# Performance work log

Measured on AMD Instinct MI355X. Metric: run time of the kernel, lower is better.

Reference implementation:

```python
import jax, jax.numpy as jnp
import numpy as np

B_AUDIOS = 64      # num audios in batch
NODES    = 2048    # 5-frame chunks (nodes) per audio
IN, HID, OUT = 512, 256, 128
HEADS, NCLS  = 2, 7
NEG_SLOPE = 0.2    # PyG GATConv default


def setup_inputs() -> dict:
    key = jax.random.key(0)
    ks = jax.random.split(key, 12)
    N = B_AUDIOS * NODES
    # chain edges within each audio: i -> i+1 (local), offset per audio
    base = np.arange(NODES - 1)
    src = (base[None, :] + np.arange(B_AUDIOS)[:, None] * NODES).reshape(-1)
    edge_index = jnp.asarray(np.stack([src, src + 1]), dtype=jnp.int32)
    batch_indices = jnp.repeat(jnp.arange(B_AUDIOS, dtype=jnp.int32), NODES)
    s = 0.05
    return {
        "x": jax.random.normal(ks[0], (N, IN), jnp.float32),
        "edge_index": edge_index,
        "batch_indices": batch_indices,
        "num_audios": B_AUDIOS,
        "W1": jax.random.normal(ks[1], (HEADS * HID, IN)) * s,
        "as1": jax.random.normal(ks[2], (HEADS, HID)) * s,
        "ad1": jax.random.normal(ks[3], (HEADS, HID)) * s,
        "b1": jnp.zeros((HID,), jnp.float32),
        "W2": jax.random.normal(ks[4], (HEADS * OUT, HID)) * s,
        "as2": jax.random.normal(ks[5], (HEADS, OUT)) * s,
        "ad2": jax.random.normal(ks[6], (HEADS, OUT)) * s,
        "b2": jnp.zeros((OUT,), jnp.float32),
        "Wt": jax.random.normal(ks[7], (1, OUT)) * s,
        "bt": jnp.zeros((1,), jnp.float32),
        "Wa": jax.random.normal(ks[8], (2, OUT)) * s,
        "ba": jnp.zeros((2,), jnp.float32),
        "Wn": jax.random.normal(ks[9], (NCLS, OUT)) * s,
        "bn": jnp.zeros((NCLS,), jnp.float32),
    }


def _seg_softmax(e, seg, n):
    m = jax.ops.segment_max(e, seg, num_segments=n)
    ex = jnp.exp(e - m[seg])
    return ex / jax.ops.segment_sum(ex, seg, num_segments=n)[seg]


def _gat_conv(x, src, dst, W, a_src, a_dst, b):
    # PyG GATConv, heads=H, concat=False (head-mean), with self loops
    N = x.shape[0]
    H, C = a_src.shape
    loops = jnp.arange(N, dtype=src.dtype)
    s = jnp.concatenate([src, loops])
    d = jnp.concatenate([dst, loops])
    h = (x @ W.T).reshape(N, H, C)                      # [N,H,C]
    al_s = jnp.einsum('nhc,hc->nh', h, a_src)           # [N,H]
    al_d = jnp.einsum('nhc,hc->nh', h, a_dst)
    e = jax.nn.leaky_relu(al_s[s] + al_d[d], NEG_SLOPE)  # [E,H]
    alpha = _seg_softmax(e, d, N)                        # softmax over in-edges of dst
    out = jax.ops.segment_sum(alpha[:, :, None] * h[s], d, num_segments=N)
    return out.mean(axis=1) + b                          # concat=False -> head mean


def reference(x, edge_index, batch_indices, num_audios,
              W1, as1, ad1, b1, W2, as2, ad2, b2,
              Wt, bt, Wa, ba, Wn, bn):
    src, dst = edge_index[0], edge_index[1]
    # global GAT (gat1 -> relu -> gat2)
    h1 = jax.nn.relu(_gat_conv(x, src, dst, W1, as1, ad1, b1))
    emb = _gat_conv(h1, src, dst, W2, as2, ad2, b2)      # [N, OUT]
    node_pred = jax.nn.softmax(emb @ Wn.T + bn, axis=-1)
    # per-audio subgraph GAT: graphs are disjoint per-audio chains, so running the
    # same GATModel on each subgraph equals restricting the global embeddings.
    logit = (emb @ Wt.T + bt)[:, 0]                      # [N]
    w = _seg_softmax(logit, batch_indices, num_audios)   # per-audio temporal softmax
    attended = jax.ops.segment_sum(w[:, None] * emb, batch_indices,
                                   num_segments=num_audios)  # [B, OUT]
    audio_pred = attended @ Wa.T + ba                    # [B, 2]
    return node_pred, audio_pred
```

## Files before the change

### kernel.cpp

```cpp
#include <hip/hip_runtime.h>
#include <hip/hip_bf16.h>

typedef __bf16 bf16x8 __attribute__((ext_vector_type(8)));
typedef float f32x4 __attribute__((ext_vector_type(4)));

#define NTOT   131072
#define NODES_PER_AUDIO 2048
#define NAUDIO 64
#define POOL_CHUNKS 16
#define CHUNK_NODES (NODES_PER_AUDIO / POOL_CHUNKS)

__global__ __launch_bounds__(256)
void detect_dtype(const unsigned* __restrict__ x, int* __restrict__ flag)
{
    const int tid = threadIdx.x;
    int cnt = 0;
    for (int i = tid; i < 4096; i += 256) {
        unsigned e = (x[i] >> 7) & 0xFF;
        cnt += (e >= 100 && e <= 145) ? 1 : 0;
    }
    __shared__ int red[256];
    red[tid] = cnt; __syncthreads();
    for (int s = 128; s > 0; s >>= 1) {
        if (tid < s) red[tid] += red[tid + s];
        __syncthreads();
    }
    if (tid == 0) *flag = (red[0] > 3000) ? 1 : 0;
}

struct W14 { const void* s[14]; int n[14]; int off[14]; };

__global__ __launch_bounds__(256)
void convert_weights(W14 w, const int* __restrict__ flag, __bf16* __restrict__ wb)
{
    const int f = *flag;
    const int stride = gridDim.x * 256;
    for (int t = 0; t < 14; t++) {
        const void* src = w.s[t];
        __bf16* d = wb + w.off[t];
        for (int i = blockIdx.x * 256 + threadIdx.x; i < w.n[t]; i += stride)
            d[i] = f ? ((const __bf16*)src)[i] : (__bf16)((const float*)src)[i];
    }
}

template<int NX, bool DYN>
__global__ __launch_bounds__(256)
void gemm_tile(const void* __restrict__ Araw, const __bf16* __restrict__ W,
               __bf16* __restrict__ C, int M, int K, int Nc,
               const int* __restrict__ flagp)
{
    __shared__ __align__(16) __bf16 As[128 * 64];
    __shared__ __align__(16) __bf16 Bs[128 * 64];

    const int nb  = gridDim.x;
    const int ny  = nb / NX;
    const int ypx = ny >> 3;
    const int bid = blockIdx.x;
    const int xcd = bid & 7;
    const int local = bid >> 3;
    const int by = xcd * ypx + local / NX;
    const int bx = local % NX;

    const int colBase = bx * 128;
    const int rowBase = by * 128;
    const int tid  = threadIdx.x;
    const int wave = tid >> 6;
    const int lane = tid & 63;
    const int wrow = (wave >> 1) * 64;
    const int wcol = (wave & 1) * 64;
    const int lr = lane & 15;
    const int lq = lane >> 4;
    int f = 1;
    if constexpr (DYN) f = *flagp;

    f32x4 acc[4][4] = {};

    const __bf16* A16 = (const __bf16*)Araw;
    const float*  A32 = (const float*)Araw;
    const __bf16* ap[4]; const float* af32[4]; const __bf16* bp[4];
    #pragma unroll
    for (int i = 0; i < 4; i++) {
        const int c = tid + 256 * i;
        const int r = c >> 3, q = c & 7;
        ap[i]   = A16 + (size_t)(rowBase + r) * K + q * 8;
        af32[i] = A32 + (size_t)(rowBase + r) * K + q * 8;
        bp[i]   = W   + (size_t)(colBase + r) * K + q * 8;
    }

    for (int k0 = 0; k0 < K; k0 += 64) {
        __syncthreads();
        #pragma unroll
        for (int i = 0; i < 4; i++) {
            const int c = tid + 256 * i;
            __builtin_amdgcn_global_load_lds(
                (const __attribute__((address_space(1))) void*)(bp[i] + k0),
                (__attribute__((address_space(3))) void*)&Bs[c * 8], 16, 0, 0);
        }
        if (!DYN || f) {
            #pragma unroll
            for (int i = 0; i < 4; i++) {
                const int c = tid + 256 * i;
                __builtin_amdgcn_global_load_lds(
                    (const __attribute__((address_space(1))) void*)(ap[i] + k0),
                    (__attribute__((address_space(3))) void*)&As[c * 8], 16, 0, 0);
            }
        } else {
            #pragma unroll
            for (int i = 0; i < 4; i++) {
                const int c = tid + 256 * i;
                float4 u0 = *(const float4*)(af32[i] + k0);
                float4 u1 = *(const float4*)(af32[i] + k0 + 4);
                __bf16 t[8] = {(__bf16)u0.x, (__bf16)u0.y, (__bf16)u0.z, (__bf16)u0.w,
                               (__bf16)u1.x, (__bf16)u1.y, (__bf16)u1.z, (__bf16)u1.w};
                *(int4*)&As[c * 8] = *(int4*)t;
            }
        }
        __syncthreads();

        #pragma unroll
        for (int kk = 0; kk < 2; kk++) {
            bf16x8 avf[4], bvf[4];
            #pragma unroll
            for (int i = 0; i < 4; i++)
                avf[i] = *(const bf16x8*)&As[(wrow + i * 16 + lr) * 64 + kk * 32 + lq * 8];
            #pragma unroll
            for (int j = 0; j < 4; j++)
                bvf[j] = *(const bf16x8*)&Bs[(wcol + j * 16 + lr) * 64 + kk * 32 + lq * 8];
            #pragma unroll
            for (int i = 0; i < 4; i++)
                #pragma unroll
                for (int j = 0; j < 4; j++)
                    acc[i][j] = __builtin_amdgcn_mfma_f32_16x16x32_bf16(
                        avf[i], bvf[j], acc[i][j], 0, 0, 0);
        }
    }

    #pragma unroll
    for (int i = 0; i < 4; i++) {
        #pragma unroll
        for (int j = 0; j < 4; j++) {
            int col = colBase + wcol + j * 16 + lr;
            #pragma unroll
            for (int r = 0; r < 4; r++) {
                int row = rowBase + wrow + i * 16 + lq * 4 + r;
                C[(size_t)row * Nc + col] = (__bf16)acc[i][j][r];
            }
        }
    }
}

template<int C, bool RELU, bool FUSE_HEAD>
__global__ __launch_bounds__(256)
void agg_fused(const __bf16* __restrict__ h, const __bf16* __restrict__ a_s,
               const __bf16* __restrict__ a_d, const __bf16* __restrict__ bias,
               void* __restrict__ outv,
               const __bf16* __restrict__ Wn, const __bf16* __restrict__ bn,
               const __bf16* __restrict__ Wt, const __bf16* __restrict__ bt,
               void* __restrict__ node_pred, float* __restrict__ logit,
               const int* __restrict__ flag)
{
    constexpr int D = 2 * C;
    constexpr int V = D / 64;
    const int n = blockIdx.x * 4 + (threadIdx.x >> 6);
    const int lane = threadIdx.x & 63;
    const bool have_prev = (n & (NODES_PER_AUDIO - 1)) != 0;
    const size_t np = have_prev ? (size_t)(n - 1) : (size_t)n;
    const int base = lane * V;

    __bf16 h0v[V], h1v[V];
    if constexpr (V == 8) {
        *(int4*)h0v = *(const int4*)(h + (size_t)n * D + base);
        *(int4*)h1v = *(const int4*)(h + np * D + base);
    } else {
        *(int2*)h0v = *(const int2*)(h + (size_t)n * D + base);
        *(int2*)h1v = *(const int2*)(h + np * D + base);
    }

    float ps = 0.f, pd = 0.f, pp = 0.f;
    #pragma unroll
    for (int j = 0; j < V; j++) {
        float av = (float)a_s[base + j], dv = (float)a_d[base + j];
        float x0 = (float)h0v[j], x1 = (float)h1v[j];
        ps += x0 * av; pd += x0 * dv; pp += x1 * av;
    }
    #pragma unroll
    for (int off = 1; off < 32; off <<= 1) {
        ps += __shfl_xor(ps, off, 64);
        pd += __shfl_xor(pd, off, 64);
        pp += __shfl_xor(pp, off, 64);
    }

    float es = ps + pd;  es = es > 0.f ? es : 0.2f * es;
    float a_self = 1.f, a_prev = 0.f;
    if (have_prev) {
        float ep = pp + pd;  ep = ep > 0.f ? ep : 0.2f * ep;
        float m = fmaxf(es, ep);
        float wsx = __expf(es - m), wpx = __expf(ep - m);
        float inv = 1.f / (wsx + wpx);
        a_self = wsx * inv; a_prev = wpx * inv;
    }

    const int cb = (lane & 31) * V;
    float outj[V];
    #pragma unroll
    for (int j = 0; j < V; j++) {
        float p = a_self * (float)h0v[j] + a_prev * (float)h1v[j];
        p = 0.5f * (p + __shfl_xor(p, 32, 64));
        p += (float)bias[cb + j];
        if (RELU) p = fmaxf(p, 0.f);
        outj[j] = p;
    }

    if constexpr (!FUSE_HEAD) {
        if (lane < 32) {
            __bf16 ov[V];
            #pragma unroll
            for (int j = 0; j < V; j++) ov[j] = (__bf16)outj[j];
            if constexpr (V == 8)
                *(int4*)((__bf16*)outv + (size_t)n * C + cb) = *(int4*)ov;
            else
                *(int2*)((__bf16*)outv + (size_t)n * C + cb) = *(int2*)ov;
        }
    } else {
        if (lane < 32)
            *(float4*)((float*)outv + (size_t)n * C + cb) = *(float4*)outj;

        float acc[8];
        #pragma unroll
        for (int k = 0; k < 7; k++) {
            float a = 0.f;
            #pragma unroll
            for (int j = 0; j < V; j++)
                a += outj[j] * (float)Wn[k * C + cb + j];
            acc[k] = a;
        }
        {
            float a = 0.f;
            #pragma unroll
            for (int j = 0; j < V; j++)
                a += outj[j] * (float)Wt[cb + j];
            acc[7] = a;
        }
        #pragma unroll
        for (int off = 1; off < 32; off <<= 1)
            #pragma unroll
            for (int k = 0; k < 8; k++)
                acc[k] += __shfl_xor(acc[k], off, 64);

        if (lane == 0) {
            float lg[7], m = -1e30f;
            #pragma unroll
            for (int k = 0; k < 7; k++) {
                lg[k] = acc[k] + (float)bn[k];
                m = fmaxf(m, lg[k]);
            }
            float s = 0.f;
            #pragma unroll
            for (int k = 0; k < 7; k++) { lg[k] = __expf(lg[k] - m); s += lg[k]; }
            float inv = 1.f / s;
            if (*flag) {
                #pragma unroll
                for (int k = 0; k < 7; k++)
                    ((__bf16*)node_pred)[(size_t)n * 7 + k] = (__bf16)(lg[k] * inv);
            } else {
                #pragma unroll
                for (int k = 0; k < 7; k++)
                    ((float*)node_pred)[(size_t)n * 7 + k] = lg[k] * inv;
            }
            logit[n] = acc[7] + (float)bt[0];
        }
    }
}

__global__ __launch_bounds__(256)
void audio_stats(const float* __restrict__ logit, float2* __restrict__ stats)
{
    const int b = blockIdx.x;
    const int tid = threadIdx.x;
    __shared__ float red[256];
    const float* lg = logit + b * NODES_PER_AUDIO;

    float m = -1e30f;
    for (int i = tid; i < NODES_PER_AUDIO; i += 256) m = fmaxf(m, lg[i]);
    red[tid] = m; __syncthreads();
    for (int s = 128; s > 0; s >>= 1) {
        if (tid < s) red[tid] = fmaxf(red[tid], red[tid + s]);
        __syncthreads();
    }
    m = red[0]; __syncthreads();

    float s = 0.f;
    for (int i = tid; i < NODES_PER_AUDIO; i += 256) s += __expf(lg[i] - m);
    red[tid] = s; __syncthreads();
    for (int st = 128; st > 0; st >>= 1) {
        if (tid < st) red[tid] += red[tid + st];
        __syncthreads();
    }
    if (tid == 0) stats[b] = make_float2(m, 1.f / red[0]);
}

__global__ __launch_bounds__(256)
void audio_partial(const float* __restrict__ emb, const float* __restrict__ logit,
                   const float2* __restrict__ stats, float* __restrict__ partial)
{
    const int b = blockIdx.x >> 4;
    const int chunk = blockIdx.x & 15;
    const int tid = threadIdx.x;
    const int c = tid & 127, half = tid >> 7;
    const float m = stats[b].x, inv = stats[b].y;
    const float* lg = logit + b * NODES_PER_AUDIO;
    const float* eb = emb + (size_t)b * NODES_PER_AUDIO * 128;

    __shared__ float attbuf[256];
    const int n0 = chunk * CHUNK_NODES + half * (CHUNK_NODES / 2);
    float att = 0.f;
    for (int i = n0; i < n0 + CHUNK_NODES / 2; i++) {
        float w = __expf(lg[i] - m) * inv;
        att += w * eb[(size_t)i * 128 + c];
    }
    attbuf[tid] = att; __syncthreads();
    if (tid < 128)
        partial[(size_t)(b * POOL_CHUNKS + chunk) * 128 + tid] =
            attbuf[tid] + attbuf[tid + 128];
}

__global__ __launch_bounds__(64)
void audio_final(const float* __restrict__ partial, const __bf16* __restrict__ Wa,
                 const __bf16* __restrict__ ba, void* __restrict__ outbase,
                 const int* __restrict__ flag)
{
    const int b = blockIdx.x;
    const int lane = threadIdx.x;
    const float* pb = partial + (size_t)b * POOL_CHUNKS * 128;

    float a0 = 0.f, a1 = 0.f;
    #pragma unroll
    for (int k = 0; k < POOL_CHUNKS; k++) {
        a0 += pb[k * 128 + lane * 2];
        a1 += pb[k * 128 + lane * 2 + 1];
    }
    float p0 = a0 * (float)Wa[lane * 2]       + a1 * (float)Wa[lane * 2 + 1];
    float p1 = a0 * (float)Wa[128 + lane * 2] + a1 * (float)Wa[128 + lane * 2 + 1];
    #pragma unroll
    for (int off = 1; off < 64; off <<= 1) {
        p0 += __shfl_xor(p0, off, 64);
        p1 += __shfl_xor(p1, off, 64);
    }
    if (lane == 0) {
        float r0 = p0 + (float)ba[0];
        float r1 = p1 + (float)ba[1];
        if (*flag) {
            ((__bf16*)outbase)[(size_t)NTOT * 7 + b * 2 + 0] = (__bf16)r0;
            ((__bf16*)outbase)[(size_t)NTOT * 7 + b * 2 + 1] = (__bf16)r1;
        } else {
            ((float*)outbase)[(size_t)NTOT * 7 + b * 2 + 0] = r0;
            ((float*)outbase)[(size_t)NTOT * 7 + b * 2 + 1] = r1;
        }
    }
}

extern "C" void kernel_launch(void* const* d_in, const int* in_sizes, int n_in,
                              void* d_out, int out_size, void* d_ws, size_t ws_size,
                              hipStream_t stream)
{
    const void* x = d_in[0];
    char* ws = (char*)d_ws;
    const size_t N = NTOT;

    __bf16* h  = (__bf16*)ws;
    size_t off = N * 1024;
    __bf16* h1 = (__bf16*)(ws + off); off += N * 512;
    float* logit = (float*)(ws + off); off += N * 4;
    __bf16* wb = (__bf16*)(ws + off); off += 331008 * 2;
    int* flag = (int*)(ws + off); off += 16;
    float2* stats = (float2*)(ws + off); off += NAUDIO * sizeof(float2);
    float* partial = (float*)(ws + off); off += (size_t)NAUDIO * POOL_CHUNKS * 128 * 4;
    __bf16* g2 = h;
    float* emb = (float*)(ws + N * 512);

    const int O_W1 = 0,      O_W2 = 262144, O_as1 = 327680, O_ad1 = 328192;
    const int O_b1 = 328704, O_as2 = 328960, O_ad2 = 329216, O_b2 = 329472;
    const int O_Wt = 329600, O_bt = 329728, O_Wa = 329736, O_ba = 329992;
    const int O_Wn = 330000, O_bn = 330896;

    W14 w;
    const void* srcs[14] = { d_in[4], d_in[8], d_in[5], d_in[6], d_in[7],
                             d_in[9], d_in[10], d_in[11], d_in[12], d_in[13],
                             d_in[14], d_in[15], d_in[16], d_in[17] };
    const int ns[14]   = { 262144, 65536, 512, 512, 256, 256, 256, 128,
                           128, 1, 256, 2, 896, 7 };
    const int offs[14] = { O_W1, O_W2, O_as1, O_ad1, O_b1, O_as2, O_ad2, O_b2,
                           O_Wt, O_bt, O_Wa, O_ba, O_Wn, O_bn };
    for (int i = 0; i < 14; i++) { w.s[i] = srcs[i]; w.n[i] = ns[i]; w.off[i] = offs[i]; }

    const int nwb = NTOT / 4;

    detect_dtype<<<1, 256, 0, stream>>>((const unsigned*)x, flag);
    convert_weights<<<512, 256, 0, stream>>>(w, flag, wb);

    gemm_tile<4, true><<<4 * (NTOT / 128), 256, 0, stream>>>(
        x, wb + O_W1, h, NTOT, 512, 512, flag);
    agg_fused<256, true, false><<<nwb, 256, 0, stream>>>(
        h, wb + O_as1, wb + O_ad1, wb + O_b1, h1,
        nullptr, nullptr, nullptr, nullptr, nullptr, nullptr, flag);
    gemm_tile<2, false><<<2 * (NTOT / 128), 256, 0, stream>>>(
        h1, wb + O_W2, g2, NTOT, 256, 256, flag);
    agg_fused<128, false, true><<<nwb, 256, 0, stream>>>(
        g2, wb + O_as2, wb + O_ad2, wb + O_b2, emb,
        wb + O_Wn, wb + O_bn, wb + O_Wt, wb + O_bt, d_out, logit, flag);
    audio_stats<<<NAUDIO, 256, 0, stream>>>(logit, stats);
    audio_partial<<<NAUDIO * POOL_CHUNKS, 256, 0, stream>>>(emb, logit, stats, partial);
    audio_final<<<NAUDIO, 64, 0, stream>>>(partial, wb + O_Wa, wb + O_ba, d_out, flag);
}
```

Baseline: 649.5 us.

## Double-buffer GEMM tiles via register staging with XOR-swizzled LDS layout

```diff
diff --git a/kernel.cpp b/kernel.cpp
--- a/kernel.cpp
+++ b/kernel.cpp
@@ -45,12 +45,12 @@
 
 template<int NX, bool DYN>
 __global__ __launch_bounds__(256)
-void gemm_tile(const void* __restrict__ Araw, const __bf16* __restrict__ W,
-               __bf16* __restrict__ C, int M, int K, int Nc,
-               const int* __restrict__ flagp)
-{
-    __shared__ __align__(16) __bf16 As[128 * 64];
-    __shared__ __align__(16) __bf16 Bs[128 * 64];
+void gemm_rs(const void* __restrict__ Araw, const __bf16* __restrict__ W,
+             __bf16* __restrict__ C, int M, int K, int Nc,
+             const int* __restrict__ flagp)
+{
+    __shared__ __align__(16) __bf16 As[2 * 128 * 64];
+    __shared__ __align__(16) __bf16 Bs[2 * 128 * 64];
 
     const int nb  = gridDim.x;
     const int ny  = nb / NX;
@@ -60,80 +60,89 @@
     const int local = bid >> 3;
     const int by = xcd * ypx + local / NX;
     const int bx = local % NX;
-
-    const int colBase = bx * 128;
-    const int rowBase = by * 128;
+    const int rowBase = by * 128, colBase = bx * 128;
+
     const int tid  = threadIdx.x;
-    const int wave = tid >> 6;
-    const int lane = tid & 63;
-    const int wrow = (wave >> 1) * 64;
-    const int wcol = (wave & 1) * 64;
-    const int lr = lane & 15;
-    const int lq = lane >> 4;
+    const int wave = tid >> 6, lane = tid & 63;
+    const int wrow = (wave >> 1) * 64, wcol = (wave & 1) * 64;
+    const int lr = lane & 15, lq = lane >> 4;
     int f = 1;
     if constexpr (DYN) f = *flagp;
 
-    f32x4 acc[4][4] = {};
-
     const __bf16* A16 = (const __bf16*)Araw;
     const float*  A32 = (const float*)Araw;
-    const __bf16* ap[4]; const float* af32[4]; const __bf16* bp[4];
+
+    const __bf16* apB[4]; const float* apF[4]; const __bf16* bpB[4]; int ld[4];
     #pragma unroll
     for (int i = 0; i < 4; i++) {
-        const int c = tid + 256 * i;
-        const int r = c >> 3, q = c & 7;
-        ap[i]   = A16 + (size_t)(rowBase + r) * K + q * 8;
-        af32[i] = A32 + (size_t)(rowBase + r) * K + q * 8;
-        bp[i]   = W   + (size_t)(colBase + r) * K + q * 8;
-    }
-
-    for (int k0 = 0; k0 < K; k0 += 64) {
-        __syncthreads();
-        #pragma unroll
-        for (int i = 0; i < 4; i++) {
-            const int c = tid + 256 * i;
-            __builtin_amdgcn_global_load_lds(
-                (const __attribute__((address_space(1))) void*)(bp[i] + k0),
-                (__attribute__((address_space(3))) void*)&Bs[c * 8], 16, 0, 0);
-        }
-        if (!DYN || f) {
-            #pragma unroll
-            for (int i = 0; i < 4; i++) {
-                const int c = tid + 256 * i;
-                __builtin_amdgcn_global_load_lds(
-                    (const __attribute__((address_space(1))) void*)(ap[i] + k0),
-                    (__attribute__((address_space(3))) void*)&As[c * 8], 16, 0, 0);
-            }
-        } else {
-            #pragma unroll
-            for (int i = 0; i < 4; i++) {
-                const int c = tid + 256 * i;
-                float4 u0 = *(const float4*)(af32[i] + k0);
-                float4 u1 = *(const float4*)(af32[i] + k0 + 4);
-                __bf16 t[8] = {(__bf16)u0.x, (__bf16)u0.y, (__bf16)u0.z, (__bf16)u0.w,
-                               (__bf16)u1.x, (__bf16)u1.y, (__bf16)u1.z, (__bf16)u1.w};
-                *(int4*)&As[c * 8] = *(int4*)t;
-            }
-        }
-        __syncthreads();
+        const int c = tid + 256 * i, r = c >> 3, q = (c & 7) ^ (r & 7);
+        apB[i] = A16 + (size_t)(rowBase + r) * K + q * 8;
+        apF[i] = A32 + (size_t)(rowBase + r) * K + q * 8;
+        bpB[i] = W   + (size_t)(colBase + r) * K + q * 8;
+        ld[i]  = c * 8;
+    }
+
+    f32x4 acc[4][4] = {};
+    const int NS = K >> 6;
+    int4 sa[4], sb[4];
+
+    #define LOADR(S) do {                                                     \
+        const int _k0 = (S) * 64;                                             \
+        _Pragma("unroll")                                                     \
+        for (int _i = 0; _i < 4; _i++) {                                      \
+            if (!DYN || f) {                                                  \
+                sa[_i] = *(const int4*)(apB[_i] + _k0);                       \
+            } else {                                                          \
+                float4 u0 = *(const float4*)(apF[_i] + _k0);                  \
+                float4 u1 = *(const float4*)(apF[_i] + _k0 + 4);              \
+                __bf16 t[8] = {(__bf16)u0.x, (__bf16)u0.y, (__bf16)u0.z,      \
+                               (__bf16)u0.w, (__bf16)u1.x, (__bf16)u1.y,      \
+                               (__bf16)u1.z, (__bf16)u1.w};                   \
+                sa[_i] = *(const int4*)t;                                     \
+            }                                                                 \
+            sb[_i] = *(const int4*)(bpB[_i] + _k0);                           \
+        } } while (0)
+
+    #define WRITER(P) do {                                                    \
+        _Pragma("unroll")                                                     \
+        for (int _i = 0; _i < 4; _i++) {                                      \
+            *(int4*)&As[(P) * 8192 + ld[_i]] = sa[_i];                        \
+            *(int4*)&Bs[(P) * 8192 + ld[_i]] = sb[_i];                        \
+        } } while (0)
+
+    LOADR(0);
+    WRITER(0);
+    __syncthreads();
+
+    for (int s = 0; s < NS; ++s) {
+        const int p = s & 1;
+        if (s + 1 < NS) LOADR(s + 1);
 
         #pragma unroll
         for (int kk = 0; kk < 2; kk++) {
-            bf16x8 avf[4], bvf[4];
-            #pragma unroll
-            for (int i = 0; i < 4; i++)
-                avf[i] = *(const bf16x8*)&As[(wrow + i * 16 + lr) * 64 + kk * 32 + lq * 8];
-            #pragma unroll
-            for (int j = 0; j < 4; j++)
-                bvf[j] = *(const bf16x8*)&Bs[(wcol + j * 16 + lr) * 64 + kk * 32 + lq * 8];
+            bf16x8 av[4], bv[4];
+            #pragma unroll
+            for (int i = 0; i < 4; i++) {
+                const int ra = wrow + i * 16 + lr;
+                av[i] = *(const bf16x8*)
+                    &As[p * 8192 + ra * 64 + (((kk * 4 + lq) ^ (ra & 7)) * 8)];
+                const int rb = wcol + i * 16 + lr;
+                bv[i] = *(const bf16x8*)
+                    &Bs[p * 8192 + rb * 64 + (((kk * 4 + lq) ^ (rb & 7)) * 8)];
+            }
             #pragma unroll
             for (int i = 0; i < 4; i++)
                 #pragma unroll
                 for (int j = 0; j < 4; j++)
                     acc[i][j] = __builtin_amdgcn_mfma_f32_16x16x32_bf16(
-                        avf[i], bvf[j], acc[i][j], 0, 0, 0);
-        }
-    }
+                        av[i], bv[j], acc[i][j], 0, 0, 0);
+        }
+
+        if (s + 1 < NS) WRITER(p ^ 1);
+        __syncthreads();
+    }
+    #undef LOADR
+    #undef WRITER
 
     #pragma unroll
     for (int i = 0; i < 4; i++) {
@@ -167,19 +176,23 @@
     const size_t np = have_prev ? (size_t)(n - 1) : (size_t)n;
     const int base = lane * V;
 
-    __bf16 h0v[V], h1v[V];
+    __bf16 h0v[V], h1v[V], asv[V], adv[V];
     if constexpr (V == 8) {
         *(int4*)h0v = *(const int4*)(h + (size_t)n * D + base);
         *(int4*)h1v = *(const int4*)(h + np * D + base);
+        *(int4*)asv = *(const int4*)(a_s + base);
+        *(int4*)adv = *(const int4*)(a_d + base);
     } else {
         *(int2*)h0v = *(const int2*)(h + (size_t)n * D + base);
         *(int2*)h1v = *(const int2*)(h + np * D + base);
+        *(int2*)asv = *(const int2*)(a_s + base);
+        *(int2*)adv = *(const int2*)(a_d + base);
     }
 
     float ps = 0.f, pd = 0.f, pp = 0.f;
     #pragma unroll
     for (int j = 0; j < V; j++) {
-        float av = (float)a_s[base + j], dv = (float)a_d[base + j];
+        float av = (float)asv[j], dv = (float)adv[j];
         float x0 = (float)h0v[j], x1 = (float)h1v[j];
         ps += x0 * av; pd += x0 * dv; pp += x1 * av;
     }
@@ -398,12 +411,12 @@
     detect_dtype<<<1, 256, 0, stream>>>((const unsigned*)x, flag);
     convert_weights<<<512, 256, 0, stream>>>(w, flag, wb);
 
-    gemm_tile<4, true><<<4 * (NTOT / 128), 256, 0, stream>>>(
+    gemm_rs<4, true><<<4 * (NTOT / 128), 256, 0, stream>>>(
         x, wb + O_W1, h, NTOT, 512, 512, flag);
     agg_fused<256, true, false><<<nwb, 256, 0, stream>>>(
         h, wb + O_as1, wb + O_ad1, wb + O_b1, h1,
         nullptr, nullptr, nullptr, nullptr, nullptr, nullptr, flag);
-    gemm_tile<2, false><<<2 * (NTOT / 128), 256, 0, stream>>>(
+    gemm_rs<2, false><<<2 * (NTOT / 128), 256, 0, stream>>>(
         h1, wb + O_W2, g2, NTOT, 256, 256, flag);
     agg_fused<128, false, true><<<nwb, 256, 0, stream>>>(
         g2, wb + O_as2, wb + O_ad2, wb + O_b2, emb,
```

Result: slower. 851.0 us (+31.0%).

## Fuse attention pooling into GAT2 aggregation with per-block online softmax partials

Applied to the files above, without the earlier changes.

```diff
diff --git a/kernel.cpp b/kernel.cpp
--- a/kernel.cpp
+++ b/kernel.cpp
@@ -7,8 +7,7 @@
 #define NTOT   131072
 #define NODES_PER_AUDIO 2048
 #define NAUDIO 64
-#define POOL_CHUNKS 16
-#define CHUNK_NODES (NODES_PER_AUDIO / POOL_CHUNKS)
+#define BLKS_PER_AUDIO 512
 
 __global__ __launch_bounds__(256)
 void detect_dtype(const unsigned* __restrict__ x, int* __restrict__ flag)
@@ -156,30 +155,36 @@
                void* __restrict__ outv,
                const __bf16* __restrict__ Wn, const __bf16* __restrict__ bn,
                const __bf16* __restrict__ Wt, const __bf16* __restrict__ bt,
-               void* __restrict__ node_pred, float* __restrict__ logit,
-               const int* __restrict__ flag)
+               void* __restrict__ node_pred, float* __restrict__ vbuf,
+               float* __restrict__ msbuf, const int* __restrict__ flag)
 {
     constexpr int D = 2 * C;
     constexpr int V = D / 64;
-    const int n = blockIdx.x * 4 + (threadIdx.x >> 6);
+    const int blk = blockIdx.x;
+    const int wave = threadIdx.x >> 6;
+    const int n = blk * 4 + wave;
     const int lane = threadIdx.x & 63;
     const bool have_prev = (n & (NODES_PER_AUDIO - 1)) != 0;
     const size_t np = have_prev ? (size_t)(n - 1) : (size_t)n;
     const int base = lane * V;
 
-    __bf16 h0v[V], h1v[V];
+    __bf16 h0v[V], h1v[V], asv[V], adv[V];
     if constexpr (V == 8) {
         *(int4*)h0v = *(const int4*)(h + (size_t)n * D + base);
         *(int4*)h1v = *(const int4*)(h + np * D + base);
+        *(int4*)asv = *(const int4*)(a_s + base);
+        *(int4*)adv = *(const int4*)(a_d + base);
     } else {
         *(int2*)h0v = *(const int2*)(h + (size_t)n * D + base);
         *(int2*)h1v = *(const int2*)(h + np * D + base);
+        *(int2*)asv = *(const int2*)(a_s + base);
+        *(int2*)adv = *(const int2*)(a_d + base);
     }
 
     float ps = 0.f, pd = 0.f, pp = 0.f;
     #pragma unroll
     for (int j = 0; j < V; j++) {
-        float av = (float)a_s[base + j], dv = (float)a_d[base + j];
+        float av = (float)asv[j], dv = (float)adv[j];
         float x0 = (float)h0v[j], x1 = (float)h1v[j];
         ps += x0 * av; pd += x0 * dv; pp += x1 * av;
     }
@@ -222,8 +227,8 @@
                 *(int2*)((__bf16*)outv + (size_t)n * C + cb) = *(int2*)ov;
         }
     } else {
-        if (lane < 32)
-            *(float4*)((float*)outv + (size_t)n * C + cb) = *(float4*)outj;
+        __shared__ float psum[4][128];
+        __shared__ float lgw[4];
 
         float acc[8];
         #pragma unroll
@@ -267,21 +272,47 @@
                 for (int k = 0; k < 7; k++)
                     ((float*)node_pred)[(size_t)n * 7 + k] = lg[k] * inv;
             }
-            logit[n] = acc[7] + (float)bt[0];
+            lgw[wave] = acc[7] + (float)bt[0];
+        }
+        __syncthreads();
+
+        const float m_b = fmaxf(fmaxf(lgw[0], lgw[1]), fmaxf(lgw[2], lgw[3]));
+        if (lane < 32) {
+            const float we = __expf(lgw[wave] - m_b);
+            #pragma unroll
+            for (int j = 0; j < V; j++)
+                psum[wave][cb + j] = we * outj[j];
+        }
+        __syncthreads();
+
+        const int tid = threadIdx.x;
+        if (tid < 128) {
+            vbuf[(size_t)blk * 128 + tid] =
+                psum[0][tid] + psum[1][tid] + psum[2][tid] + psum[3][tid];
+        } else if (tid == 128) {
+            const float s_b = __expf(lgw[0] - m_b) + __expf(lgw[1] - m_b)
+                            + __expf(lgw[2] - m_b) + __expf(lgw[3] - m_b);
+            msbuf[(size_t)blk * 2]     = m_b;
+            msbuf[(size_t)blk * 2 + 1] = s_b;
         }
     }
 }
 
 __global__ __launch_bounds__(256)
-void audio_stats(const float* __restrict__ logit, float2* __restrict__ stats)
+void audio_comb(const float* __restrict__ vbuf, const float* __restrict__ msbuf,
+                const __bf16* __restrict__ Wa, const __bf16* __restrict__ ba,
+                void* __restrict__ outbase, const int* __restrict__ flag)
 {
     const int b = blockIdx.x;
     const int tid = threadIdx.x;
     __shared__ float red[256];
-    const float* lg = logit + b * NODES_PER_AUDIO;
+    __shared__ float ew[BLKS_PER_AUDIO];
+    __shared__ float att[128];
+    const int base = b * BLKS_PER_AUDIO;
 
     float m = -1e30f;
-    for (int i = tid; i < NODES_PER_AUDIO; i += 256) m = fmaxf(m, lg[i]);
+    for (int k = tid; k < BLKS_PER_AUDIO; k += 256)
+        m = fmaxf(m, msbuf[(size_t)(base + k) * 2]);
     red[tid] = m; __syncthreads();
     for (int s = 128; s > 0; s >>= 1) {
         if (tid < s) red[tid] = fmaxf(red[tid], red[tid + s]);
@@ -290,71 +321,48 @@
     m = red[0]; __syncthreads();
 
     float s = 0.f;
-    for (int i = tid; i < NODES_PER_AUDIO; i += 256) s += __expf(lg[i] - m);
+    for (int k = tid; k < BLKS_PER_AUDIO; k += 256) {
+        const float e = __expf(msbuf[(size_t)(base + k) * 2] - m);
+        ew[k] = e;
+        s += e * msbuf[(size_t)(base + k) * 2 + 1];
+    }
     red[tid] = s; __syncthreads();
     for (int st = 128; st > 0; st >>= 1) {
         if (tid < st) red[tid] += red[tid + st];
         __syncthreads();
     }
-    if (tid == 0) stats[b] = make_float2(m, 1.f / red[0]);
-}
-
-__global__ __launch_bounds__(256)
-void audio_partial(const float* __restrict__ emb, const float* __restrict__ logit,
-                   const float2* __restrict__ stats, float* __restrict__ partial)
-{
-    const int b = blockIdx.x >> 4;
-    const int chunk = blockIdx.x & 15;
-    const int tid = threadIdx.x;
+    const float invS = 1.f / red[0];
+    __syncthreads();
+
     const int c = tid & 127, half = tid >> 7;
-    const float m = stats[b].x, inv = stats[b].y;
-    const float* lg = logit + b * NODES_PER_AUDIO;
-    const float* eb = emb + (size_t)b * NODES_PER_AUDIO * 128;
-
-    __shared__ float attbuf[256];
-    const int n0 = chunk * CHUNK_NODES + half * (CHUNK_NODES / 2);
-    float att = 0.f;
-    for (int i = n0; i < n0 + CHUNK_NODES / 2; i++) {
-        float w = __expf(lg[i] - m) * inv;
-        att += w * eb[(size_t)i * 128 + c];
-    }
-    attbuf[tid] = att; __syncthreads();
-    if (tid < 128)
-        partial[(size_t)(b * POOL_CHUNKS + chunk) * 128 + tid] =
-            attbuf[tid] + attbuf[tid + 128];
-}
-
-__global__ __launch_bounds__(64)
-void audio_final(const float* __restrict__ partial, const __bf16* __restrict__ Wa,
-                 const __bf16* __restrict__ ba, void* __restrict__ outbase,
-                 const int* __restrict__ flag)
-{
-    const int b = blockIdx.x;
-    const int lane = threadIdx.x;
-    const float* pb = partial + (size_t)b * POOL_CHUNKS * 128;
-
-    float a0 = 0.f, a1 = 0.f;
-    #pragma unroll
-    for (int k = 0; k < POOL_CHUNKS; k++) {
-        a0 += pb[k * 128 + lane * 2];
-        a1 += pb[k * 128 + lane * 2 + 1];
-    }
-    float p0 = a0 * (float)Wa[lane * 2]       + a1 * (float)Wa[lane * 2 + 1];
-    float p1 = a0 * (float)Wa[128 + lane * 2] + a1 * (float)Wa[128 + lane * 2 + 1];
-    #pragma unroll
-    for (int off = 1; off < 64; off <<= 1) {
-        p0 += __shfl_xor(p0, off, 64);
-        p1 += __shfl_xor(p1, off, 64);
-    }
-    if (lane == 0) {
-        float r0 = p0 + (float)ba[0];
-        float r1 = p1 + (float)ba[1];
-        if (*flag) {
-            ((__bf16*)outbase)[(size_t)NTOT * 7 + b * 2 + 0] = (__bf16)r0;
-            ((__bf16*)outbase)[(size_t)NTOT * 7 + b * 2 + 1] = (__bf16)r1;
-        } else {
-            ((float*)outbase)[(size_t)NTOT * 7 + b * 2 + 0] = r0;
-            ((float*)outbase)[(size_t)NTOT * 7 + b * 2 + 1] = r1;
+    float a = 0.f;
+    const int k0 = half * (BLKS_PER_AUDIO / 2);
+    for (int k = k0; k < k0 + BLKS_PER_AUDIO / 2; ++k)
+        a += ew[k] * vbuf[(size_t)(base + k) * 128 + c];
+    red[tid] = a; __syncthreads();
+    if (tid < 128) att[tid] = (red[tid] + red[tid + 128]) * invS;
+    __syncthreads();
+
+    if (tid < 64) {
+        const int lane = tid;
+        const float a0 = att[lane * 2], a1 = att[lane * 2 + 1];
+        float p0 = a0 * (float)Wa[lane * 2]       + a1 * (float)Wa[lane * 2 + 1];
+        float p1 = a0 * (float)Wa[128 + lane * 2] + a1 * (float)Wa[128 + lane * 2 + 1];
+        #pragma unroll
+        for (int off = 1; off < 64; off <<= 1) {
+            p0 += __shfl_xor(p0, off, 64);
+            p1 += __shfl_xor(p1, off, 64);
+        }
+        if (lane == 0) {
+            const float r0 = p0 + (float)ba[0];
+            const float r1 = p1 + (float)ba[1];
+            if (*flag) {
+                ((__bf16*)outbase)[(size_t)NTOT * 7 + b * 2 + 0] = (__bf16)r0;
+                ((__bf16*)outbase)[(size_t)NTOT * 7 + b * 2 + 1] = (__bf16)r1;
+            } else {
+                ((float*)outbase)[(size_t)NTOT * 7 + b * 2 + 0] = r0;
+                ((float*)outbase)[(size_t)NTOT * 7 + b * 2 + 1] = r1;
+            }
         }
     }
 }
@@ -370,13 +378,12 @@
     __bf16* h  = (__bf16*)ws;
     size_t off = N * 1024;
     __bf16* h1 = (__bf16*)(ws + off); off += N * 512;
-    float* logit = (float*)(ws + off); off += N * 4;
     __bf16* wb = (__bf16*)(ws + off); off += 331008 * 2;
     int* flag = (int*)(ws + off); off += 16;
-    float2* stats = (float2*)(ws + off); off += NAUDIO * sizeof(float2);
-    float* partial = (float*)(ws + off); off += (size_t)NAUDIO * POOL_CHUNKS * 128 * 4;
+    off = (off + 255) & ~(size_t)255;
+    float* vbuf  = (float*)(ws + off); off += (size_t)(NTOT / 4) * 128 * 4;
+    float* msbuf = (float*)(ws + off); off += (size_t)(NTOT / 4) * 2 * 4;
     __bf16* g2 = h;
-    float* emb = (float*)(ws + N * 512);
 
     const int O_W1 = 0,      O_W2 = 262144, O_as1 = 327680, O_ad1 = 328192;
     const int O_b1 = 328704, O_as2 = 328960, O_ad2 = 329216, O_b2 = 329472;
@@ -402,13 +409,12 @@
         x, wb + O_W1, h, NTOT, 512, 512, flag);
     agg_fused<256, true, false><<<nwb, 256, 0, stream>>>(
         h, wb + O_as1, wb + O_ad1, wb + O_b1, h1,
-        nullptr, nullptr, nullptr, nullptr, nullptr, nullptr, flag);
+        nullptr, nullptr, nullptr, nullptr, nullptr, nullptr, nullptr, flag);
     gemm_tile<2, false><<<2 * (NTOT / 128), 256, 0, stream>>>(
         h1, wb + O_W2, g2, NTOT, 256, 256, flag);
     agg_fused<128, false, true><<<nwb, 256, 0, stream>>>(
-        g2, wb + O_as2, wb + O_ad2, wb + O_b2, emb,
-        wb + O_Wn, wb + O_bn, wb + O_Wt, wb + O_bt, d_out, logit, flag);
-    audio_stats<<<NAUDIO, 256, 0, stream>>>(logit, stats);
-    audio_partial<<<NAUDIO * POOL_CHUNKS, 256, 0, stream>>>(emb, logit, stats, partial);
-    audio_final<<<NAUDIO, 64, 0, stream>>>(partial, wb + O_Wa, wb + O_ba, d_out, flag);
-}
+        g2, wb + O_as2, wb + O_ad2, wb + O_b2, nullptr,
+        wb + O_Wn, wb + O_bn, wb + O_Wt, wb + O_bt, d_out, vbuf, msbuf, flag);
+    audio_comb<<<NAUDIO, 256, 0, stream>>>(vbuf, msbuf, wb + O_Wa, wb + O_ba,
+                                           d_out, flag);
+}
```

New measurement: 698.2 us. +7.5%, slower.
